# Performance work log

Measured on AMD Instinct MI355X. Metric: run time of the kernel, lower is better.

The kernel has to match this reference:

```python
import jax, jax.numpy as jnp
import numpy as np

N = 40000
E = 640000
D_IN = 128
H = 8
C = 16  # out_dim per head


def setup_inputs() -> dict:
    key = jax.random.key(0)
    ks = jax.random.split(key, 7)
    features = jax.random.normal(ks[0], (N, D_IN), dtype=jnp.float32)
    edge_index = jax.random.randint(ks[1], (2, E), 0, N, dtype=jnp.int32)
    edge_weight = jax.random.uniform(ks[2], (E,), dtype=jnp.float32)
    # xavier-ish scales
    W_lin = jax.random.normal(ks[3], (D_IN, H * C), dtype=jnp.float32) * (1.0 / np.sqrt(D_IN))
    att_l = jax.random.normal(ks[4], (1, H, C), dtype=jnp.float32) * 0.1
    att_r = jax.random.normal(ks[5], (1, H, C), dtype=jnp.float32) * 0.1
    W_res = jax.random.normal(ks[6], (D_IN, H * C), dtype=jnp.float32) * (1.0 / np.sqrt(D_IN))
    return {"features": features, "edge_index": edge_index, "edge_weight": edge_weight,
            "W_lin": W_lin, "att_l": att_l, "att_r": att_r, "W_res": W_res}


def _segment_softmax(logits, seg, num_segments):
    # logits: (E, H), seg: (E,) destination node ids
    m = jax.ops.segment_max(logits, seg, num_segments=num_segments)  # (N, H)
    ex = jnp.exp(logits - m[seg])
    s = jax.ops.segment_sum(ex, seg, num_segments=num_segments)  # (N, H)
    return ex / s[seg]


def reference(features, edge_index, edge_weight, W_lin, att_l, att_r, W_res):
    src, dst = edge_index[0], edge_index[1]
    x = (features @ W_lin).reshape(-1, H, C)              # (N, H, C)
    alpha_l = (x * att_l).sum(-1)                          # (N, H)
    alpha_r = (x * att_r).sum(-1)                          # (N, H)
    alpha = alpha_l[src] + alpha_r[dst]                    # (E, H)
    alpha = edge_weight[:, None] * alpha
    alpha = jnp.where(alpha >= 0, alpha, 0.2 * alpha)      # leaky_relu(0.2)
    coef = _segment_softmax(alpha, dst, N)                 # (E, H)
    msgs = x[src] * coef[:, :, None]                       # (E, H, C)
    agg = jax.ops.segment_sum(msgs, dst, num_segments=N)   # (N, H, C)
    out = jax.nn.elu(agg).reshape(-1, H * C)
    out = out + features @ W_res
    return out
```

## Files before the change

### kernel.cpp

```cpp
#include <hip/hip_runtime.h>
#include <math.h>

#define N_NODES 40000
#define N_EDGES 640000
#define D 128
#define H 8
#define C 16
#define NBG 1250
#define KP 136
#define NBUCK 625
#define NCH 512
#define ECH 1250
#define MAXB 1536

typedef __attribute__((ext_vector_type(8))) short short8;
typedef __attribute__((ext_vector_type(4))) float floatx4;


__device__ __forceinline__ unsigned short f2bf(float f) {
  const unsigned u = __float_as_uint(f);
  return (unsigned short)((u + 0x7FFFu + ((u >> 16) & 1u)) >> 16);
}
__device__ __forceinline__ float bflo(unsigned p) {
  return __uint_as_float(p << 16);
}
__device__ __forceinline__ float bfhi(unsigned p) {
  return __uint_as_float(p & 0xFFFF0000u);
}
__device__ __forceinline__ float bf2f(unsigned short u) {
  return __uint_as_float((unsigned)u << 16);
}

__global__ void k_prep(const float* __restrict__ Wlin,
                       const float* __restrict__ Wres,
                       unsigned short* __restrict__ wt)
{
  const int n = blockIdx.x, k = threadIdx.x, g = blockIdx.y;
  const float* W = g ? Wres : Wlin;
  wt[((g * 128 + n) * 128) + k] = f2bf(W[(long)k * 128 + n]);
}

__global__ __launch_bounds__(256, 4) void k_gemm(
    const float* __restrict__ feat, const unsigned short* __restrict__ wt,
    unsigned short* __restrict__ xh, float* __restrict__ outp,
    const float* __restrict__ attl, const float* __restrict__ attr,
    float* __restrict__ al, float* __restrict__ ar,
    const int* __restrict__ dst, int* __restrict__ pk, int* __restrict__ cnt2)
{
  __shared__ short sA[32 * KP];
  __shared__ float sD[32 * 132];
  const int t = threadIdx.x;

  if (blockIdx.y == 1) {
    if (blockIdx.x >= NCH) return;
    int* lcnt = (int*)sA;
    for (int i = t; i < NBUCK; i += 256) lcnt[i] = 0;
    __syncthreads();
    const int c = blockIdx.x, e0 = c * ECH;
    for (int e = e0 + t; e < e0 + ECH; e += 256) {
      const int d = dst[e];
      const int r = atomicAdd(&lcnt[d >> 6], 1);
      pk[e] = ((d >> 6) << 17) | ((d & 63) << 11) | r;
    }
    __syncthreads();
    for (int i = t; i < NBUCK; i += 256) cnt2[c * NBUCK + i] = lcnt[i];
    return;
  }

  const int row0 = blockIdx.x * 32;

  {
    const int kq = t & 31;
    const int rb = (t >> 5) * 4;
    #pragma unroll
    for (int i = 0; i < 4; ++i) {
      const int r = rb + i;
      const float4 f = *(const float4*)&feat[(long)(row0 + r) * 128 + kq * 4];
      const unsigned lo = (unsigned)f2bf(f.x) | ((unsigned)f2bf(f.y) << 16);
      const unsigned hi = (unsigned)f2bf(f.z) | ((unsigned)f2bf(f.w) << 16);
      *(uint2*)&sA[r * KP + kq * 4] = make_uint2(lo, hi);
    }
  }

  const int w = t >> 6, lane = t & 63;
  const int c15 = lane & 15, q = lane >> 4;

  short8 bfr0[4][2], bfr1[4][2];
  #pragma unroll
  for (int kc = 0; kc < 4; ++kc)
    #pragma unroll
    for (int nt = 0; nt < 2; ++nt) {
      const int n = (w * 2 + nt) * 16 + c15;
      bfr0[kc][nt] = *(const short8*)&wt[n * 128 + kc * 32 + q * 8];
      bfr1[kc][nt] = *(const short8*)&wt[16384 + n * 128 + kc * 32 + q * 8];
    }
  __syncthreads();

  floatx4 acc0[2][2], acc1[2][2];
  #pragma unroll
  for (int mt = 0; mt < 2; ++mt)
    #pragma unroll
    for (int nt = 0; nt < 2; ++nt) {
      acc0[mt][nt] = (floatx4){0.f, 0.f, 0.f, 0.f};
      acc1[mt][nt] = (floatx4){0.f, 0.f, 0.f, 0.f};
    }
  #pragma unroll
  for (int kc = 0; kc < 4; ++kc)
    #pragma unroll
    for (int mt = 0; mt < 2; ++mt) {
      const short8 afr = *(const short8*)&sA[(mt * 16 + c15) * KP + kc * 32 + q * 8];
      acc0[mt][0] = __builtin_amdgcn_mfma_f32_16x16x32_bf16(afr, bfr0[kc][0], acc0[mt][0], 0, 0, 0);
      acc0[mt][1] = __builtin_amdgcn_mfma_f32_16x16x32_bf16(afr, bfr0[kc][1], acc0[mt][1], 0, 0, 0);
      acc1[mt][0] = __builtin_amdgcn_mfma_f32_16x16x32_bf16(afr, bfr1[kc][0], acc1[mt][0], 0, 0, 0);
      acc1[mt][1] = __builtin_amdgcn_mfma_f32_16x16x32_bf16(afr, bfr1[kc][1], acc1[mt][1], 0, 0, 0);
    }

  const int orow = t >> 3, seg = t & 7;
  const int grow = row0 + orow;

  #pragma unroll
  for (int mt = 0; mt < 2; ++mt)
    #pragma unroll
    for (int nt = 0; nt < 2; ++nt) {
      const int col = (w * 2 + nt) * 16 + c15;
      #pragma unroll
      for (int r = 0; r < 4; ++r)
        sD[(mt * 16 + q * 4 + r) * 132 + col] = acc0[mt][nt][r];
    }
  __syncthreads();
  {
    #pragma unroll
    for (int i = 0; i < 2; ++i) {
      const float4 v0 = *(const float4*)&sD[orow * 132 + seg * 16 + i * 8];
      const float4 v1 = *(const float4*)&sD[orow * 132 + seg * 16 + i * 8 + 4];
      uint4 u;
      u.x = (unsigned)f2bf(v0.x) | ((unsigned)f2bf(v0.y) << 16);
      u.y = (unsigned)f2bf(v0.z) | ((unsigned)f2bf(v0.w) << 16);
      u.z = (unsigned)f2bf(v1.x) | ((unsigned)f2bf(v1.y) << 16);
      u.w = (unsigned)f2bf(v1.z) | ((unsigned)f2bf(v1.w) << 16);
      *(uint4*)&xh[(long)grow * 128 + seg * 16 + i * 8] = u;
    }
    const int h = seg;
    float sl = 0.f, sr = 0.f;
    #pragma unroll
    for (int c4 = 0; c4 < 4; ++c4) {
      const float4 xv = *(const float4*)&sD[orow * 132 + h * 16 + c4 * 4];
      const float4 lv = *(const float4*)&attl[h * 16 + c4 * 4];
      const float4 rv = *(const float4*)&attr[h * 16 + c4 * 4];
      sl += xv.x * lv.x + xv.y * lv.y + xv.z * lv.z + xv.w * lv.w;
      sr += xv.x * rv.x + xv.y * rv.y + xv.z * rv.z + xv.w * rv.w;
    }
    al[(long)grow * 8 + h] = sl;
    ar[(long)grow * 8 + h] = sr;
  }
  __syncthreads();

  #pragma unroll
  for (int mt = 0; mt < 2; ++mt)
    #pragma unroll
    for (int nt = 0; nt < 2; ++nt) {
      const int col = (w * 2 + nt) * 16 + c15;
      #pragma unroll
      for (int r = 0; r < 4; ++r)
        sD[(mt * 16 + q * 4 + r) * 132 + col] = acc1[mt][nt][r];
    }
  __syncthreads();
  #pragma unroll
  for (int i = 0; i < 4; ++i) {
    const float4 v = *(const float4*)&sD[orow * 132 + seg * 16 + i * 4];
    *(float4*)&outp[(long)grow * 128 + seg * 16 + i * 4] = v;
  }
}

__global__ __launch_bounds__(512) void k_scan2a(
    const int* __restrict__ cnt2, int* __restrict__ pre2T, int* __restrict__ total)
{
  __shared__ int sd[NCH];
  const int b = blockIdx.x;
  const int t = threadIdx.x;
  const int v = cnt2[t * NBUCK + b];
  sd[t] = v;
  __syncthreads();
  #pragma unroll
  for (int off = 1; off < NCH; off <<= 1) {
    const int add = (t >= off) ? sd[t - off] : 0;
    __syncthreads();
    sd[t] += add;
    __syncthreads();
  }
  pre2T[b * NCH + t] = sd[t] - v;
  if (t == NCH - 1) total[b] = sd[t];
}

__global__ __launch_bounds__(256) void k_place(
    const int* __restrict__ pk, const int* __restrict__ src,
    const float* __restrict__ ew,
    const int* __restrict__ pre2T, uint2* __restrict__ einfo)
{
  const int e = blockIdx.x * 256 + threadIdx.x;
  if (e >= N_EDGES) return;
  const int k = pk[e];
  const int b = k >> 17, dl = (k >> 11) & 63, r = k & 2047;
  const int c = e / ECH;
  const int p = b * MAXB + pre2T[b * NCH + c] + r;
  einfo[p] = make_uint2(((unsigned)src[e] << 6) | (unsigned)dl,
                        __float_as_uint(ew[e]));
}

__global__ __launch_bounds__(1024, 4) void k_edgeagg(
    const int* __restrict__ total, const uint2* __restrict__ einfo,
    const float* __restrict__ al, const float* __restrict__ ar,
    const unsigned short* __restrict__ xh, float* __restrict__ outp)
{
  __shared__ uint2 sE[MAXB];
  __shared__ unsigned short sP[MAXB * 8];
  __shared__ int sS[MAXB];
  __shared__ float sAr[512];
  __shared__ int bcnt[64], bbase[64], bpos[64];
  const int b = blockIdx.x;
  const int cntb = total[b];
  const int t = threadIdx.x;
  if (t < 64) bcnt[t] = 0;
  if (t < 512) sAr[t] = ar[((long)(b << 6)) * 8 + t];
  __syncthreads();
  const long e0 = (long)b * MAXB;
  for (int i = t; i < cntb; i += 1024) {
    const uint2 m = einfo[e0 + i];
    sE[i] = m;
    atomicAdd(&bcnt[m.x & 63], 1);
  }
  __syncthreads();
  if (t < 64) {
    const int v = bcnt[t];
    int incl = v;
    #pragma unroll
    for (int off = 1; off < 64; off <<= 1) {
      const int n = __shfl_up(incl, off, 64);
      if (t >= off) incl += n;
    }
    bbase[t] = incl - v;
    bpos[t] = 0;
  }
  __syncthreads();
  for (int i = t; i < cntb; i += 1024) {
    const uint2 m = sE[i];
    const int dl = m.x & 63;
    const int s = (int)(m.x >> 6);
    const float w = __uint_as_float(m.y);
    const float4 l0 = *(const float4*)&al[(long)s * 8];
    const float4 l1 = *(const float4*)&al[(long)s * 8 + 4];
    const float* arr = &sAr[dl * 8];
    float lv[8] = {l0.x + arr[0], l0.y + arr[1], l0.z + arr[2], l0.w + arr[3],
                   l1.x + arr[4], l1.y + arr[5], l1.z + arr[6], l1.w + arr[7]};
    #pragma unroll
    for (int h = 0; h < 8; ++h) {
      float a = w * lv[h];
      a = (a >= 0.f) ? a : 0.2f * a;
      lv[h] = __expf(a);
    }
    const int r = atomicAdd(&bpos[dl], 1);
    const int qq = bbase[dl] + r;
    sS[qq] = s;
    uint4 u;
    u.x = (unsigned)f2bf(lv[0]) | ((unsigned)f2bf(lv[1]) << 16);
    u.y = (unsigned)f2bf(lv[2]) | ((unsigned)f2bf(lv[3]) << 16);
    u.z = (unsigned)f2bf(lv[4]) | ((unsigned)f2bf(lv[5]) << 16);
    u.w = (unsigned)f2bf(lv[6]) | ((unsigned)f2bf(lv[7]) << 16);
    *(uint4*)&sP[qq * 8] = u;
  }
  __syncthreads();

  const int wv = t >> 6, lane = t & 63;
  const int h = lane >> 3;
  const int co = lane * 2;
  #pragma unroll
  for (int j = 0; j < 4; ++j) {
    const int dl = wv * 4 + j;
    const int start = bbase[dl];
    const int end = start + bcnt[dl];
    if (end <= start) continue;

    float2 a0 = {0.f, 0.f}, a1 = {0.f, 0.f}, a2 = {0.f, 0.f}, a3 = {0.f, 0.f};
    float s0s = 0.f, s1s = 0.f, s2s = 0.f, s3s = 0.f;
    int p = start;
    for (; p + 4 <= end; p += 4) {
      const int s0 = sS[p + 0], s1 = sS[p + 1];
      const int s2 = sS[p + 2], s3 = sS[p + 3];
      const float e0v = bf2f(sP[(p + 0) * 8 + h]);
      const float e1v = bf2f(sP[(p + 1) * 8 + h]);
      const float e2v = bf2f(sP[(p + 2) * 8 + h]);
      const float e3v = bf2f(sP[(p + 3) * 8 + h]);
      const unsigned v0 = *(const unsigned*)&xh[(long)s0 * 128 + co];
      const unsigned v1 = *(const unsigned*)&xh[(long)s1 * 128 + co];
      const unsigned v2 = *(const unsigned*)&xh[(long)s2 * 128 + co];
      const unsigned v3 = *(const unsigned*)&xh[(long)s3 * 128 + co];
      a0.x = fmaf(bflo(v0), e0v, a0.x); a0.y = fmaf(bfhi(v0), e0v, a0.y); s0s += e0v;
      a1.x = fmaf(bflo(v1), e1v, a1.x); a1.y = fmaf(bfhi(v1), e1v, a1.y); s1s += e1v;
      a2.x = fmaf(bflo(v2), e2v, a2.x); a2.y = fmaf(bfhi(v2), e2v, a2.y); s2s += e2v;
      a3.x = fmaf(bflo(v3), e3v, a3.x); a3.y = fmaf(bfhi(v3), e3v, a3.y); s3s += e3v;
    }
    for (; p < end; ++p) {
      const int s = sS[p];
      const float ev = bf2f(sP[p * 8 + h]);
      const unsigned v = *(const unsigned*)&xh[(long)s * 128 + co];
      a0.x = fmaf(bflo(v), ev, a0.x);
      a0.y = fmaf(bfhi(v), ev, a0.y);
      s0s += ev;
    }
    const float rs = 1.0f / ((s0s + s1s) + (s2s + s3s));
    const float ax = ((a0.x + a1.x) + (a2.x + a3.x)) * rs;
    const float ay = ((a0.y + a1.y) + (a2.y + a3.y)) * rs;

    const long dnode = (long)(b << 6) + dl;
    float2 o = *(float2*)&outp[dnode * 128 + co];
    o.x += (ax > 0.f) ? ax : expm1f(ax);
    o.y += (ay > 0.f) ? ay : expm1f(ay);
    *(float2*)&outp[dnode * 128 + co] = o;
  }
}

extern "C" void kernel_launch(void* const* d_in, const int* in_sizes, int n_in,
                              void* d_out, int out_size, void* d_ws, size_t ws_size,
                              hipStream_t stream) {
  const float* feat = (const float*)d_in[0];
  const int*   eidx = (const int*)d_in[1];
  const float* ew   = (const float*)d_in[2];
  const float* Wlin = (const float*)d_in[3];
  const float* attl = (const float*)d_in[4];
  const float* attr = (const float*)d_in[5];
  const float* Wres = (const float*)d_in[6];
  float* outp = (float*)d_out;

  float* ws = (float*)d_ws;
  unsigned short* xh = (unsigned short*)ws;
  float* al   = ws + 5120000;
  float* ar   = ws + 5440000;
  int*   pk   = (int*)(ws + 5760000);
  uint2* einfo = (uint2*)(ws + 6500000);
  int*   cnt2 = (int*)(ws + 8500000);
  int*   pre2T = (int*)(ws + 8900000);
  int*   total = (int*)(ws + 9300000);
  unsigned short* wt = (unsigned short*)(ws + 12800000);

  const int* src = eidx;
  const int* dst = eidx + N_EDGES;

  dim3 pgrid(128, 2);
  k_prep<<<pgrid, 128, 0, stream>>>(Wlin, Wres, wt);
  dim3 ggrid(NBG, 2);
  k_gemm<<<ggrid, 256, 0, stream>>>(feat, wt, xh, outp, attl, attr, al, ar,
                                    dst, pk, cnt2);
  k_scan2a<<<NBUCK, NCH, 0, stream>>>(cnt2, pre2T, total);
  k_place<<<N_EDGES / 256, 256, 0, stream>>>(pk, src, ew, pre2T, einfo);
  k_edgeagg<<<NBUCK, 1024, 0, stream>>>(total, einfo, al, ar, xh, outp);
}
```

Baseline: 157.0 us.

## Bin edges into fixed-capacity per-chunk slots with overflow list, dropping scan and place kernels

The bucketing pass now writes each edge's packed payload straight into a fixed-capacity slot region indexed by (bucket, chunk, rank). Edges beyond the capacity of 12 go to a global overflow list. This removes the prefix-scan and placement kernels and the intermediate packed-key buffer. The aggregation kernel now walks all slots of its bucket, compacting the valid ones through a shared-memory atomic, and then scans the overflow list. The cost is sparser einfo reads, a per-block pass over the overflow list, and edge order that changes from run to run. Edges are silently dropped if more than 4096 overflow.

```diff
diff --git a/kernel.cpp b/kernel.cpp
--- a/kernel.cpp
+++ b/kernel.cpp
@@ -11,7 +11,10 @@
 #define NBUCK 625
 #define NCH 512
 #define ECH 1250
+#define CAP 12
+#define SLOTS (NCH * CAP)
 #define MAXB 1536
+#define OVCAP 4096
 
 typedef __attribute__((ext_vector_type(8))) short short8;
 typedef __attribute__((ext_vector_type(4))) float floatx4;
@@ -33,9 +36,10 @@
 
 __global__ void k_prep(const float* __restrict__ Wlin,
                        const float* __restrict__ Wres,
-                       unsigned short* __restrict__ wt)
+                       unsigned short* __restrict__ wt, int* __restrict__ ovfn)
 {
   const int n = blockIdx.x, k = threadIdx.x, g = blockIdx.y;
+  if (n == 0 && g == 0 && k == 0) *ovfn = 0;
   const float* W = g ? Wres : Wlin;
   wt[((g * 128 + n) * 128) + k] = f2bf(W[(long)k * 128 + n]);
 }
@@ -45,7 +49,9 @@
     unsigned short* __restrict__ xh, float* __restrict__ outp,
     const float* __restrict__ attl, const float* __restrict__ attr,
     float* __restrict__ al, float* __restrict__ ar,
-    const int* __restrict__ dst, int* __restrict__ pk, int* __restrict__ cnt2)
+    const int* __restrict__ src, const int* __restrict__ dst,
+    const float* __restrict__ ew, uint2* __restrict__ einfo,
+    int* __restrict__ cnt2, int* __restrict__ ovfn, uint4* __restrict__ ovf)
 {
   __shared__ short sA[32 * KP];
   __shared__ float sD[32 * 132];
@@ -59,8 +65,18 @@
     const int c = blockIdx.x, e0 = c * ECH;
     for (int e = e0 + t; e < e0 + ECH; e += 256) {
       const int d = dst[e];
-      const int r = atomicAdd(&lcnt[d >> 6], 1);
-      pk[e] = ((d >> 6) << 17) | ((d & 63) << 11) | r;
+      const int b = d >> 6, dl = d & 63;
+      const int r = atomicAdd(&lcnt[b], 1);
+      const unsigned pay = ((unsigned)src[e] << 6) | (unsigned)dl;
+      const unsigned wbits = __float_as_uint(ew[e]);
+      if (r < CAP) {
+        einfo[((long)b * NCH + c) * CAP + r] = make_uint2(pay, wbits);
+      } else {
+        const int oi = atomicAdd(ovfn, 1);
+        if (oi < OVCAP)
+          ovf[oi] = make_uint4((unsigned)b, (unsigned)dl,
+                               (unsigned)src[e], wbits);
+      }
     }
     __syncthreads();
     for (int i = t; i < NBUCK; i += 256) cnt2[c * NBUCK + i] = lcnt[i];
@@ -172,43 +188,9 @@
   }
 }
 
-__global__ __launch_bounds__(512) void k_scan2a(
-    const int* __restrict__ cnt2, int* __restrict__ pre2T, int* __restrict__ total)
-{
-  __shared__ int sd[NCH];
-  const int b = blockIdx.x;
-  const int t = threadIdx.x;
-  const int v = cnt2[t * NBUCK + b];
-  sd[t] = v;
-  __syncthreads();
-  #pragma unroll
-  for (int off = 1; off < NCH; off <<= 1) {
-    const int add = (t >= off) ? sd[t - off] : 0;
-    __syncthreads();
-    sd[t] += add;
-    __syncthreads();
-  }
-  pre2T[b * NCH + t] = sd[t] - v;
-  if (t == NCH - 1) total[b] = sd[t];
-}
-
-__global__ __launch_bounds__(256) void k_place(
-    const int* __restrict__ pk, const int* __restrict__ src,
-    const float* __restrict__ ew,
-    const int* __restrict__ pre2T, uint2* __restrict__ einfo)
-{
-  const int e = blockIdx.x * 256 + threadIdx.x;
-  if (e >= N_EDGES) return;
-  const int k = pk[e];
-  const int b = k >> 17, dl = (k >> 11) & 63, r = k & 2047;
-  const int c = e / ECH;
-  const int p = b * MAXB + pre2T[b * NCH + c] + r;
-  einfo[p] = make_uint2(((unsigned)src[e] << 6) | (unsigned)dl,
-                        __float_as_uint(ew[e]));
-}
-
 __global__ __launch_bounds__(1024, 4) void k_edgeagg(
-    const int* __restrict__ total, const uint2* __restrict__ einfo,
+    const int* __restrict__ cnt2, const uint2* __restrict__ einfo,
+    const int* __restrict__ ovfn, const uint4* __restrict__ ovf,
     const float* __restrict__ al, const float* __restrict__ ar,
     const unsigned short* __restrict__ xh, float* __restrict__ outp)
 {
@@ -216,20 +198,40 @@
   __shared__ unsigned short sP[MAXB * 8];
   __shared__ int sS[MAXB];
   __shared__ float sAr[512];
+  __shared__ int scnt[NCH];
   __shared__ int bcnt[64], bbase[64], bpos[64];
+  __shared__ int nE;
   const int b = blockIdx.x;
-  const int cntb = total[b];
   const int t = threadIdx.x;
   if (t < 64) bcnt[t] = 0;
+  if (t == 64) nE = 0;
   if (t < 512) sAr[t] = ar[((long)(b << 6)) * 8 + t];
-  __syncthreads();
-  const long e0 = (long)b * MAXB;
-  for (int i = t; i < cntb; i += 1024) {
-    const uint2 m = einfo[e0 + i];
-    sE[i] = m;
-    atomicAdd(&bcnt[m.x & 63], 1);
-  }
-  __syncthreads();
+  else scnt[t - 512] = min(cnt2[(t - 512) * NBUCK + b], CAP);
+  __syncthreads();
+
+  const long base = (long)b * SLOTS;
+  for (int i = t; i < SLOTS; i += 1024) {
+    const int c = i / CAP;
+    const int r = i - c * CAP;
+    if (r < scnt[c]) {
+      const uint2 m = einfo[base + i];
+      const int k = atomicAdd(&nE, 1);
+      sE[k] = m;
+      atomicAdd(&bcnt[m.x & 63], 1);
+    }
+  }
+  const int no = *ovfn;
+  for (int i = t; i < no; i += 1024) {
+    const uint4 o = ovf[i];
+    if ((int)o.x == b) {
+      const int k = atomicAdd(&nE, 1);
+      sE[k] = make_uint2((o.z << 6) | o.y, o.w);
+      atomicAdd(&bcnt[o.y], 1);
+    }
+  }
+  __syncthreads();
+  const int cntb = nE;
+
   if (t < 64) {
     const int v = bcnt[t];
     int incl = v;
@@ -242,6 +244,7 @@
     bpos[t] = 0;
   }
   __syncthreads();
+
   for (int i = t; i < cntb; i += 1024) {
     const uint2 m = sE[i];
     const int dl = m.x & 63;
@@ -335,22 +338,20 @@
   unsigned short* xh = (unsigned short*)ws;
   float* al   = ws + 5120000;
   float* ar   = ws + 5440000;
-  int*   pk   = (int*)(ws + 5760000);
-  uint2* einfo = (uint2*)(ws + 6500000);
-  int*   cnt2 = (int*)(ws + 8500000);
-  int*   pre2T = (int*)(ws + 8900000);
-  int*   total = (int*)(ws + 9300000);
-  unsigned short* wt = (unsigned short*)(ws + 12800000);
+  uint2* einfo = (uint2*)(ws + 6000000);
+  int*   cnt2 = (int*)(ws + 14000000);
+  int*   ovfn = (int*)(ws + 14400000);
+  uint4* ovf  = (uint4*)(ws + 14400064);
+  unsigned short* wt = (unsigned short*)(ws + 15000000);
 
   const int* src = eidx;
   const int* dst = eidx + N_EDGES;
 
   dim3 pgrid(128, 2);
-  k_prep<<<pgrid, 128, 0, stream>>>(Wlin, Wres, wt);
+  k_prep<<<pgrid, 128, 0, stream>>>(Wlin, Wres, wt, ovfn);
   dim3 ggrid(NBG, 2);
   k_gemm<<<ggrid, 256, 0, stream>>>(feat, wt, xh, outp, attl, attr, al, ar,
-                                    dst, pk, cnt2);
-  k_scan2a<<<NBUCK, NCH, 0, stream>>>(cnt2, pre2T, total);
-  k_place<<<N_EDGES / 256, 256, 0, stream>>>(pk, src, ew, pre2T, einfo);
-  k_edgeagg<<<NBUCK, 1024, 0, stream>>>(total, einfo, al, ar, xh, outp);
-}
+                                    src, dst, ew, einfo, cnt2, ovfn, ovf);
+  k_edgeagg<<<NBUCK, 1024, 0, stream>>>(cnt2, einfo, ovfn, ovf, al, ar,
+                                        xh, outp);
+}
```

Result: faster. 150.0 us (-4.5%).
